# Performance work log

Hardware: AMD Instinct MI355X
Metric: run time of the kernel (lower is better)

## Reference

```python
import jax, jax.numpy as jnp
import numpy as np

B, N, CIN, H, UNITS = 8, 2048, 256, 256, 256


def setup_inputs() -> dict:
    key = jax.random.key(0)
    ks = jax.random.split(key, 7)
    s = 1.0 / np.sqrt(CIN)
    return {
        "x": jax.random.normal(ks[0], (B, N, CIN), dtype=jnp.float32),
        "Wq": jax.random.normal(ks[1], (CIN, H), dtype=jnp.float32) * s,
        "bq": jax.random.normal(ks[2], (H,), dtype=jnp.float32) * 0.01,
        "Wk": jax.random.normal(ks[3], (CIN, H), dtype=jnp.float32) * s,
        "bk": jax.random.normal(ks[4], (H,), dtype=jnp.float32) * 0.01,
        "Wm": jax.random.normal(ks[5], (H, UNITS), dtype=jnp.float32) * (1.0 / np.sqrt(H)),
        "bm": jax.random.normal(ks[6], (UNITS,), dtype=jnp.float32) * 0.01,
    }


def reference(x, Wq, bq, Wk, bk, Wm, bm):
    # Dense projections with fused relu (as in the Keras module)
    q = jax.nn.relu(x @ Wq + bq)          # (B,N,H)
    k = jax.nn.relu(x @ Wk + bk)          # (B,N,H)
    v = q                                 # NOTE: source uses fc_query for value (fc_value unused)
    # Unscaled key @ query^T, softmax over last axis
    kq = jax.nn.softmax(jnp.einsum('bnh,bmh->bnm', k, q), axis=-1)  # (B,N,N)
    # value^T @ kq, then Permute((2,1)): att[b,m,h] = sum_n v[b,n,h] * kq[b,n,m]
    att = jnp.einsum('bnh,bnm->bmh', v, kq)                          # (B,N,H)
    return jax.nn.relu(att @ Wm + bm)                                # (B,N,UNITS)
```

## Files before the change

### kernel.cpp

```cpp
#include <hip/hip_runtime.h>
#include <hip/hip_bf16.h>
#include <math.h>

#define BB   8
#define NN   2048
#define CC   256
#define MTOT (BB * NN)

typedef __bf16 bf16_t;
typedef bf16_t    bf16x8 __attribute__((ext_vector_type(8)));
typedef _Float16  halfx8 __attribute__((ext_vector_type(8)));
typedef float     floatx4 __attribute__((ext_vector_type(4)));

#define LOG2E 1.44269504088896f

__device__ __forceinline__ void gl_lds16(const bf16_t* g, bf16_t* l) {
    __builtin_amdgcn_global_load_lds(
        (const __attribute__((address_space(1))) unsigned int*)g,
        (__attribute__((address_space(3))) unsigned int*)l, 16, 0, 0);
}

template<int OMODE, bool BIASRELU, bool DO_STATS>
__global__ __launch_bounds__(256, 3)
void gemm_nt(const bf16_t* __restrict__ A, const bf16_t* __restrict__ B,
             void* __restrict__ C, const float* __restrict__ bias,
             int lda, int ldb, int ldc,
             long strideA, long strideB, long strideC,
             float* __restrict__ pm, float* __restrict__ pl)
{
    const int b = blockIdx.z;
    A += (long)b * strideA;
    B += (long)b * strideB;
    const int m0 = blockIdx.y * 128;
    const int n0 = blockIdx.x * 128;

    __shared__ bf16_t As[128 * 32];
    __shared__ bf16_t Bs[128 * 32];
    __shared__ float  smx[4][4][16];
    __shared__ float  ssm[4][4][16];

    const int tid  = threadIdx.x;
    const int wid  = tid >> 6, lane = tid & 63;
    const int wm   = (wid >> 1) * 64, wn = (wid & 1) * 64;
    const int fr   = lane & 15;
    const int kb   = (lane >> 4) * 8;

    floatx4 acc[4][4] = {};

    for (int k0 = 0; k0 < 256; k0 += 32) {
#pragma unroll
        for (int r = 0; r < 2; ++r) {
            const int lin = tid + r * 256;
            const int rw  = lin >> 2, kc = lin & 3;
            gl_lds16(A + (long)(m0 + rw) * lda + k0 + kc * 8, As + lin * 8);
            gl_lds16(B + (long)(n0 + rw) * ldb + k0 + kc * 8, Bs + lin * 8);
        }
        __syncthreads();
        bf16x8 af[4], bf[4];
#pragma unroll
        for (int f = 0; f < 4; ++f) {
            af[f] = *(const bf16x8*)(As + (wm + f * 16 + fr) * 32 + kb);
            bf[f] = *(const bf16x8*)(Bs + (wn + f * 16 + fr) * 32 + kb);
        }
#pragma unroll
        for (int f = 0; f < 4; ++f)
#pragma unroll
            for (int g = 0; g < 4; ++g)
                acc[f][g] = __builtin_amdgcn_mfma_f32_16x16x32_bf16(af[f], bf[g], acc[f][g], 0, 0, 0);
        __syncthreads();
    }

    const int rbase = (lane >> 4) * 4;
#pragma unroll
    for (int g = 0; g < 4; ++g) {
        const int n = n0 + wn + g * 16 + fr;
        const float bv = BIASRELU ? bias[n] : 0.0f;
#pragma unroll
        for (int f = 0; f < 4; ++f) {
#pragma unroll
            for (int r = 0; r < 4; ++r) {
                const int m = m0 + wm + f * 16 + rbase + r;
                float v = acc[f][g][r] + bv;
                if (BIASRELU) v = v > 0.0f ? v : 0.0f;
                if (OMODE == 0)
                    ((float*)C)[(long)b * strideC + (long)m * ldc + n] = v;
                else if (OMODE == 1)
                    ((bf16_t*)C)[(long)b * strideC + (long)m * ldc + n] = (bf16_t)v;
                else
                    ((_Float16*)C)[(long)b * strideC + (long)m * ldc + n] = (_Float16)v;
            }
        }
    }

    if (DO_STATS) {
        float lmax[4], lsum[4];
#pragma unroll
        for (int g = 0; g < 4; ++g) {
            float m = -1e30f;
#pragma unroll
            for (int f = 0; f < 4; ++f)
#pragma unroll
                for (int r = 0; r < 4; ++r) m = fmaxf(m, acc[f][g][r]);
            m = fmaxf(m, __shfl_xor(m, 16));
            m = fmaxf(m, __shfl_xor(m, 32));
            float s = 0.0f;
#pragma unroll
            for (int f = 0; f < 4; ++f)
#pragma unroll
                for (int r = 0; r < 4; ++r) s += __expf(acc[f][g][r] - m);
            s += __shfl_xor(s, 16);
            s += __shfl_xor(s, 32);
            lmax[g] = m; lsum[g] = s;
        }
        if (lane < 16) {
#pragma unroll
            for (int g = 0; g < 4; ++g) {
                smx[wid][g][lane] = lmax[g];
                ssm[wid][g][lane] = lsum[g];
            }
        }
        __syncthreads();
        if (tid < 128) {
            const int pair = tid >> 6;
            const int idx  = tid & 63;
            const int g = idx >> 4, f2 = idx & 15;
            const float m0v = smx[pair][g][f2], m1v = smx[pair + 2][g][f2];
            const float M = fmaxf(m0v, m1v);
            const float L = ssm[pair][g][f2] * __expf(m0v - M) +
                            ssm[pair + 2][g][f2] * __expf(m1v - M);
            const int n = n0 + pair * 64 + g * 16 + f2;
            const long o = ((long)b * 16 + blockIdx.y) * NN + n;
            pm[o] = M;
            pl[o] = L;
        }
    }
}

__global__ __launch_bounds__(256)
void stats_combine(const float* __restrict__ pm, const float* __restrict__ pl,
                   float* __restrict__ c2)
{
    const int i = blockIdx.x * 256 + threadIdx.x;
    const int b = i >> 11, n = i & 2047;
    float M = -1e30f, L = 0.0f;
#pragma unroll
    for (int t = 0; t < 16; ++t) {
        const long o = ((long)b * 16 + t) * NN + n;
        const float m = pm[o], l = pl[o];
        const float nm = fmaxf(M, m);
        L = L * __expf(M - nm) + l * __expf(m - nm);
        M = nm;
    }
    c2[i] = (M + logf(L)) * LOG2E;
}

#define APAD 68
__global__ __launch_bounds__(256, 4)
void att_out(const _Float16* __restrict__ St, const bf16_t* __restrict__ qmT,
             const float* __restrict__ c2, const float* __restrict__ bm,
             float* __restrict__ out)
{
    const int b  = blockIdx.z;
    const int m0 = blockIdx.x * 32;
    const int u0 = blockIdx.y * 128;
    const _Float16* S  = St  + (long)b * NN * NN;
    const bf16_t*   Q  = qmT + (long)b * 256 * NN;
    const float*    C2 = c2  + b * NN;
    float*          O  = out + (long)b * NN * 256;

    __shared__ bf16_t As[32 * APAD];
    __shared__ bf16_t Bs[128 * 64];

    const int tid  = threadIdx.x;
    const int wid  = tid >> 6, lane = tid & 63;
    const int wm2  = (wid >> 1) * 16;
    const int wu   = (wid & 1) * 64;
    const int fr   = lane & 15;
    const int u16  = lane >> 4;
    const int kb   = u16 * 8;
    const int fsw  = fr & 7;
    const int arow = tid >> 3;
    const int aseg = tid & 7;

    const _Float16* Srow = S + (long)(m0 + arow) * NN + aseg * 8;

    floatx4 acc[4] = {};

    for (int n0 = 0; n0 < NN; n0 += 64) {
#pragma unroll
        for (int r = 0; r < 4; ++r) {
            const int lin = tid + r * 256;
            const int rw  = lin >> 3, kc = lin & 7;
            const int kcs = kc ^ (rw & 7);
            gl_lds16(Q + (long)(u0 + rw) * NN + n0 + kcs * 8, Bs + lin * 8);
        }
        const halfx8 hv = *(const halfx8*)(Srow + n0);
        const float4 ca = *(const float4*)(C2 + n0 + aseg * 8);
        const float4 cb = *(const float4*)(C2 + n0 + aseg * 8 + 4);
        bf16x8 p;
        p[0] = (bf16_t)exp2f(fmaf((float)hv[0], LOG2E, -ca.x));
        p[1] = (bf16_t)exp2f(fmaf((float)hv[1], LOG2E, -ca.y));
        p[2] = (bf16_t)exp2f(fmaf((float)hv[2], LOG2E, -ca.z));
        p[3] = (bf16_t)exp2f(fmaf((float)hv[3], LOG2E, -ca.w));
        p[4] = (bf16_t)exp2f(fmaf((float)hv[4], LOG2E, -cb.x));
        p[5] = (bf16_t)exp2f(fmaf((float)hv[5], LOG2E, -cb.y));
        p[6] = (bf16_t)exp2f(fmaf((float)hv[6], LOG2E, -cb.z));
        p[7] = (bf16_t)exp2f(fmaf((float)hv[7], LOG2E, -cb.w));
        *(bf16x8*)(As + arow * APAD + aseg * 8) = p;
        __syncthreads();

        bf16x8 af[2], bg[4][2];
#pragma unroll
        for (int j = 0; j < 2; ++j)
            af[j] = *(const bf16x8*)(As + (wm2 + fr) * APAD + j * 32 + kb);
#pragma unroll
        for (int g = 0; g < 4; ++g)
#pragma unroll
            for (int j = 0; j < 2; ++j) {
                const int chunk = (j * 4 + u16) ^ fsw;
                bg[g][j] = *(const bf16x8*)(Bs + (wu + g * 16 + fr) * 64 + chunk * 8);
            }
#pragma unroll
        for (int j = 0; j < 2; ++j)
#pragma unroll
            for (int g = 0; g < 4; ++g)
                acc[g] = __builtin_amdgcn_mfma_f32_16x16x32_bf16(af[j], bg[g][j], acc[g], 0, 0, 0);
        __syncthreads();
    }

    const int rbase = u16 * 4;
#pragma unroll
    for (int g = 0; g < 4; ++g) {
        const int u = u0 + wu + g * 16 + fr;
        const float bvv = bm[u];
#pragma unroll
        for (int r = 0; r < 4; ++r) {
            const int m = m0 + wm2 + rbase + r;
            const float v = acc[g][r] + bvv;
            O[(long)m * 256 + u] = v > 0.0f ? v : 0.0f;
        }
    }
}

__global__ __launch_bounds__(256)
void cvt_bf16(const float* __restrict__ x, bf16_t* __restrict__ y)
{
    const long i = ((long)blockIdx.x * 256 + threadIdx.x) * 8;
    const float4 a = *(const float4*)(x + i);
    const float4 b = *(const float4*)(x + i + 4);
    bf16x8 o;
    o[0] = (bf16_t)a.x; o[1] = (bf16_t)a.y; o[2] = (bf16_t)a.z; o[3] = (bf16_t)a.w;
    o[4] = (bf16_t)b.x; o[5] = (bf16_t)b.y; o[6] = (bf16_t)b.z; o[7] = (bf16_t)b.w;
    *(bf16x8*)(y + i) = o;
}

__global__ __launch_bounds__(256)
void prep_w(const float* __restrict__ Wq, const float* __restrict__ Wk,
            const float* __restrict__ Wm, const float* __restrict__ bq,
            const float* __restrict__ bk, bf16_t* __restrict__ WqkT,
            bf16_t* __restrict__ WmT, float* __restrict__ bqk)
{
    const int z = blockIdx.z;
    const float* W = (z == 0) ? Wq : (z == 1) ? Wk : Wm;
    bf16_t* Wt = (z == 0) ? WqkT : (z == 1) ? (WqkT + 256 * 256) : WmT;
    __shared__ float t[32][33];
    const int n0 = blockIdx.x * 32, k0 = blockIdx.y * 32;
    const int tx = threadIdx.x & 31, ty = threadIdx.x >> 5;
    for (int i = ty; i < 32; i += 8) t[i][tx] = W[(k0 + i) * 256 + n0 + tx];
    __syncthreads();
    for (int i = ty; i < 32; i += 8) Wt[(n0 + i) * 256 + k0 + tx] = (bf16_t)t[tx][i];
    if (z == 0 && blockIdx.x == 0 && blockIdx.y == 0) {
        bqk[threadIdx.x]       = bq[threadIdx.x];
        bqk[256 + threadIdx.x] = bk[threadIdx.x];
    }
}

extern "C" void kernel_launch(void* const* d_in, const int* in_sizes, int n_in,
                              void* d_out, int out_size, void* d_ws, size_t ws_size,
                              hipStream_t stream)
{
    (void)in_sizes; (void)n_in; (void)out_size; (void)ws_size;
    const float* x  = (const float*)d_in[0];
    const float* Wq = (const float*)d_in[1];
    const float* bq = (const float*)d_in[2];
    const float* Wk = (const float*)d_in[3];
    const float* bk = (const float*)d_in[4];
    const float* Wm = (const float*)d_in[5];
    const float* bm = (const float*)d_in[6];
    float* out = (float*)d_out;

    char* w = (char*)d_ws;
    _Float16* St   = (_Float16*)w;                  w += (size_t)BB * NN * NN * 2;
    bf16_t* x_bf   = (bf16_t*)w;                    w += (size_t)MTOT * 256 * 2;
    bf16_t* qk     = (bf16_t*)w;                    w += (size_t)MTOT * 512 * 2;
    bf16_t* qmT    = (bf16_t*)w;                    w += (size_t)MTOT * 256 * 2;
    bf16_t* WqkT   = (bf16_t*)w;                    w += 512 * 256 * 2;
    bf16_t* WmT    = (bf16_t*)w;                    w += 256 * 256 * 2;
    float*  bqk    = (float*)w;                     w += 512 * 4;
    float*  pm     = (float*)w;                     w += (size_t)BB * 16 * NN * 4;
    float*  pl     = (float*)w;                     w += (size_t)BB * 16 * NN * 4;
    float*  c2b    = (float*)w;

    cvt_bf16<<<dim3(MTOT * 256 / (256 * 8)), 256, 0, stream>>>(x, x_bf);
    prep_w<<<dim3(8, 8, 3), 256, 0, stream>>>(Wq, Wk, Wm, bq, bk, WqkT, WmT, bqk);

    gemm_nt<1, true, false><<<dim3(4, 128, 1), 256, 0, stream>>>(
        x_bf, WqkT, qk, bqk, 256, 256, 512, 0, 0, 0, nullptr, nullptr);

    gemm_nt<1, false, false><<<dim3(16, 2, BB), 256, 0, stream>>>(
        WmT, qk, qmT, nullptr, 256, 512, NN,
        0, (long)NN * 512, (long)256 * NN, nullptr, nullptr);

    gemm_nt<2, false, true><<<dim3(16, 16, BB), 256, 0, stream>>>(
        qk, qk + 256, St, nullptr, 512, 512, NN,
        (long)NN * 512, (long)NN * 512, (long)NN * NN, pm, pl);

    stats_combine<<<dim3(MTOT / 256), 256, 0, stream>>>(pm, pl, c2b);

    att_out<<<dim3(64, 2, BB), 256, 0, stream>>>(St, qmT, c2b, bm, out);
}
```

Baseline: 179.6 us.

## Double-buffer att_out LDS tiles and double the row tile per block

New measurement: 184.8 us. 2.9% more time.

```diff
diff --git a/kernel.cpp b/kernel.cpp
--- a/kernel.cpp
+++ b/kernel.cpp
@@ -155,25 +155,25 @@
 }
 
 #define APAD 68
-__global__ __launch_bounds__(256, 4)
+__global__ __launch_bounds__(256, 3)
 void att_out(const _Float16* __restrict__ St, const bf16_t* __restrict__ qmT,
              const float* __restrict__ c2, const float* __restrict__ bm,
              float* __restrict__ out)
 {
     const int b  = blockIdx.z;
-    const int m0 = blockIdx.x * 32;
+    const int m0 = blockIdx.x * 64;
     const int u0 = blockIdx.y * 128;
     const _Float16* S  = St  + (long)b * NN * NN;
     const bf16_t*   Q  = qmT + (long)b * 256 * NN;
     const float*    C2 = c2  + b * NN;
     float*          O  = out + (long)b * NN * 256;
 
-    __shared__ bf16_t As[32 * APAD];
-    __shared__ bf16_t Bs[128 * 64];
+    __shared__ bf16_t As[2][64 * APAD];
+    __shared__ bf16_t Bs[2][128 * 64];
 
     const int tid  = threadIdx.x;
     const int wid  = tid >> 6, lane = tid & 63;
-    const int wm2  = (wid >> 1) * 16;
+    const int wm2  = (wid >> 1) * 32;
     const int wu   = (wid & 1) * 64;
     const int fr   = lane & 15;
     const int u16  = lane >> 4;
@@ -182,49 +182,85 @@
     const int arow = tid >> 3;
     const int aseg = tid & 7;
 
-    const _Float16* Srow = S + (long)(m0 + arow) * NN + aseg * 8;
-
-    floatx4 acc[4] = {};
-
-    for (int n0 = 0; n0 < NN; n0 += 64) {
+    const _Float16* S0 = S + (long)(m0 + arow) * NN + aseg * 8;
+    const _Float16* S1 = S0 + (long)32 * NN;
+    const float*    CA = C2 + aseg * 8;
+
+    floatx4 acc[2][4] = {};
+
+    halfx8 hv0, hv1;
+    float4 ca, cb;
+
+    auto loadA = [&](int n0) {
+        hv0 = *(const halfx8*)(S0 + n0);
+        hv1 = *(const halfx8*)(S1 + n0);
+        ca  = *(const float4*)(CA + n0);
+        cb  = *(const float4*)(CA + n0 + 4);
+    };
+    auto stageB = [&](int buf, int n0) {
 #pragma unroll
         for (int r = 0; r < 4; ++r) {
             const int lin = tid + r * 256;
             const int rw  = lin >> 3, kc = lin & 7;
             const int kcs = kc ^ (rw & 7);
-            gl_lds16(Q + (long)(u0 + rw) * NN + n0 + kcs * 8, Bs + lin * 8);
-        }
-        const halfx8 hv = *(const halfx8*)(Srow + n0);
-        const float4 ca = *(const float4*)(C2 + n0 + aseg * 8);
-        const float4 cb = *(const float4*)(C2 + n0 + aseg * 8 + 4);
-        bf16x8 p;
-        p[0] = (bf16_t)exp2f(fmaf((float)hv[0], LOG2E, -ca.x));
-        p[1] = (bf16_t)exp2f(fmaf((float)hv[1], LOG2E, -ca.y));
-        p[2] = (bf16_t)exp2f(fmaf((float)hv[2], LOG2E, -ca.z));
-        p[3] = (bf16_t)exp2f(fmaf((float)hv[3], LOG2E, -ca.w));
-        p[4] = (bf16_t)exp2f(fmaf((float)hv[4], LOG2E, -cb.x));
-        p[5] = (bf16_t)exp2f(fmaf((float)hv[5], LOG2E, -cb.y));
-        p[6] = (bf16_t)exp2f(fmaf((float)hv[6], LOG2E, -cb.z));
-        p[7] = (bf16_t)exp2f(fmaf((float)hv[7], LOG2E, -cb.w));
-        *(bf16x8*)(As + arow * APAD + aseg * 8) = p;
-        __syncthreads();
-
-        bf16x8 af[2], bg[4][2];
-#pragma unroll
-        for (int j = 0; j < 2; ++j)
-            af[j] = *(const bf16x8*)(As + (wm2 + fr) * APAD + j * 32 + kb);
+            gl_lds16(Q + (long)(u0 + rw) * NN + n0 + kcs * 8, &Bs[buf][lin * 8]);
+        }
+    };
+    auto packA = [&](int buf) {
+        bf16x8 p0, p1;
+        p0[0] = (bf16_t)exp2f(fmaf((float)hv0[0], LOG2E, -ca.x));
+        p0[1] = (bf16_t)exp2f(fmaf((float)hv0[1], LOG2E, -ca.y));
+        p0[2] = (bf16_t)exp2f(fmaf((float)hv0[2], LOG2E, -ca.z));
+        p0[3] = (bf16_t)exp2f(fmaf((float)hv0[3], LOG2E, -ca.w));
+        p0[4] = (bf16_t)exp2f(fmaf((float)hv0[4], LOG2E, -cb.x));
+        p0[5] = (bf16_t)exp2f(fmaf((float)hv0[5], LOG2E, -cb.y));
+        p0[6] = (bf16_t)exp2f(fmaf((float)hv0[6], LOG2E, -cb.z));
+        p0[7] = (bf16_t)exp2f(fmaf((float)hv0[7], LOG2E, -cb.w));
+        p1[0] = (bf16_t)exp2f(fmaf((float)hv1[0], LOG2E, -ca.x));
+        p1[1] = (bf16_t)exp2f(fmaf((float)hv1[1], LOG2E, -ca.y));
+        p1[2] = (bf16_t)exp2f(fmaf((float)hv1[2], LOG2E, -ca.z));
+        p1[3] = (bf16_t)exp2f(fmaf((float)hv1[3], LOG2E, -ca.w));
+        p1[4] = (bf16_t)exp2f(fmaf((float)hv1[4], LOG2E, -cb.x));
+        p1[5] = (bf16_t)exp2f(fmaf((float)hv1[5], LOG2E, -cb.y));
+        p1[6] = (bf16_t)exp2f(fmaf((float)hv1[6], LOG2E, -cb.z));
+        p1[7] = (bf16_t)exp2f(fmaf((float)hv1[7], LOG2E, -cb.w));
+        *(bf16x8*)(&As[buf][arow * APAD + aseg * 8])        = p0;
+        *(bf16x8*)(&As[buf][(arow + 32) * APAD + aseg * 8]) = p1;
+    };
+
+    loadA(0);
+    stageB(0, 0);
+    packA(0);
+    __syncthreads();
+
+    for (int it = 0; it < NN / 64; ++it) {
+        const int cur = it & 1;
+        if (it + 1 < NN / 64) {
+            loadA((it + 1) * 64);
+            stageB(cur ^ 1, (it + 1) * 64);
+        }
+        bf16x8 af[2][2], bg[4][2];
+#pragma unroll
+        for (int f = 0; f < 2; ++f)
+#pragma unroll
+            for (int j = 0; j < 2; ++j)
+                af[f][j] = *(const bf16x8*)(&As[cur][(wm2 + f * 16 + fr) * APAD + j * 32 + kb]);
 #pragma unroll
         for (int g = 0; g < 4; ++g)
 #pragma unroll
             for (int j = 0; j < 2; ++j) {
                 const int chunk = (j * 4 + u16) ^ fsw;
-                bg[g][j] = *(const bf16x8*)(Bs + (wu + g * 16 + fr) * 64 + chunk * 8);
+                bg[g][j] = *(const bf16x8*)(&Bs[cur][(wu + g * 16 + fr) * 64 + chunk * 8]);
             }
 #pragma unroll
         for (int j = 0; j < 2; ++j)
 #pragma unroll
-            for (int g = 0; g < 4; ++g)
-                acc[g] = __builtin_amdgcn_mfma_f32_16x16x32_bf16(af[j], bg[g][j], acc[g], 0, 0, 0);
+            for (int f = 0; f < 2; ++f)
+#pragma unroll
+                for (int g = 0; g < 4; ++g)
+                    acc[f][g] = __builtin_amdgcn_mfma_f32_16x16x32_bf16(af[f][j], bg[g][j], acc[f][g], 0, 0, 0);
+        if (it + 1 < NN / 64)
+            packA(cur ^ 1);
         __syncthreads();
     }
 
@@ -234,11 +270,13 @@
         const int u = u0 + wu + g * 16 + fr;
         const float bvv = bm[u];
 #pragma unroll
-        for (int r = 0; r < 4; ++r) {
-            const int m = m0 + wm2 + rbase + r;
-            const float v = acc[g][r] + bvv;
-            O[(long)m * 256 + u] = v > 0.0f ? v : 0.0f;
-        }
+        for (int f = 0; f < 2; ++f)
+#pragma unroll
+            for (int r = 0; r < 4; ++r) {
+                const int m = m0 + wm2 + f * 16 + rbase + r;
+                const float v = acc[f][g][r] + bvv;
+                O[(long)m * 256 + u] = v > 0.0f ? v : 0.0f;
+            }
     }
 }
 
@@ -317,5 +355,5 @@
 
     stats_combine<<<dim3(MTOT / 256), 256, 0, stream>>>(pm, pl, c2b);
 
-    att_out<<<dim3(64, 2, BB), 256, 0, stream>>>(St, qmT, c2b, bm, out);
-}
+    att_out<<<dim3(32, 2, BB), 256, 0, stream>>>(St, qmT, c2b, bm, out);
+}
```

## Pipeline att_out with triple-buffered B tiles and a larger 64-row M tile

Applied to the files above, without the earlier changes.

Result: slower. 199.2 us (+10.9%).

```diff
diff --git a/kernel.cpp b/kernel.cpp
--- a/kernel.cpp
+++ b/kernel.cpp
@@ -155,25 +155,99 @@
 }
 
 #define APAD 68
-__global__ __launch_bounds__(256, 4)
+
+#define LA_(t, s) { \
+    hA0_##s = *(const halfx8*)(S0 + (long)(t) * 64); \
+    hA1_##s = *(const halfx8*)(S1 + (long)(t) * 64); \
+    cA_##s  = *(const float4*)(CA + (t) * 64); \
+    cB_##s  = *(const float4*)(CA + (t) * 64 + 4); }
+
+#define SB_(bufofs, t) { \
+    _Pragma("unroll") \
+    for (int r = 0; r < 4; ++r) { \
+        const int lin = tid + r * 256; \
+        const int rw = lin >> 3, kc = lin & 7; \
+        const int kcs = kc ^ (rw & 7); \
+        gl_lds16(Q + (long)(u0 + rw) * NN + (t) * 64 + kcs * 8, \
+                 Bs + (bufofs) + lin * 8); } }
+
+#define PACKA_(aofs, s) { \
+    bf16x8 p0, p1; \
+    p0[0] = (bf16_t)exp2f(fmaf((float)hA0_##s[0], LOG2E, -cA_##s.x)); \
+    p0[1] = (bf16_t)exp2f(fmaf((float)hA0_##s[1], LOG2E, -cA_##s.y)); \
+    p0[2] = (bf16_t)exp2f(fmaf((float)hA0_##s[2], LOG2E, -cA_##s.z)); \
+    p0[3] = (bf16_t)exp2f(fmaf((float)hA0_##s[3], LOG2E, -cA_##s.w)); \
+    p0[4] = (bf16_t)exp2f(fmaf((float)hA0_##s[4], LOG2E, -cB_##s.x)); \
+    p0[5] = (bf16_t)exp2f(fmaf((float)hA0_##s[5], LOG2E, -cB_##s.y)); \
+    p0[6] = (bf16_t)exp2f(fmaf((float)hA0_##s[6], LOG2E, -cB_##s.z)); \
+    p0[7] = (bf16_t)exp2f(fmaf((float)hA0_##s[7], LOG2E, -cB_##s.w)); \
+    p1[0] = (bf16_t)exp2f(fmaf((float)hA1_##s[0], LOG2E, -cA_##s.x)); \
+    p1[1] = (bf16_t)exp2f(fmaf((float)hA1_##s[1], LOG2E, -cA_##s.y)); \
+    p1[2] = (bf16_t)exp2f(fmaf((float)hA1_##s[2], LOG2E, -cA_##s.z)); \
+    p1[3] = (bf16_t)exp2f(fmaf((float)hA1_##s[3], LOG2E, -cA_##s.w)); \
+    p1[4] = (bf16_t)exp2f(fmaf((float)hA1_##s[4], LOG2E, -cB_##s.x)); \
+    p1[5] = (bf16_t)exp2f(fmaf((float)hA1_##s[5], LOG2E, -cB_##s.y)); \
+    p1[6] = (bf16_t)exp2f(fmaf((float)hA1_##s[6], LOG2E, -cB_##s.z)); \
+    p1[7] = (bf16_t)exp2f(fmaf((float)hA1_##s[7], LOG2E, -cB_##s.w)); \
+    *(bf16x8*)(As + (aofs) + arow * APAD + aseg * 8)        = p0; \
+    *(bf16x8*)(As + (aofs) + (arow + 32) * APAD + aseg * 8) = p1; }
+
+#define ITER_(it, sI, sP) { \
+    const int t2 = (it) + 2 < 32 ? (it) + 2 : 31; \
+    LA_(t2, sI); \
+    SB_(bstg * 8192, t2); \
+    const bf16_t* asr = As + ((it) & 1) * (64 * APAD); \
+    const bf16_t* bsr = Bs + bcur * 8192; \
+    bf16x8 af[2][2], bg[4][2]; \
+    _Pragma("unroll") \
+    for (int f = 0; f < 2; ++f) \
+        _Pragma("unroll") \
+        for (int j = 0; j < 2; ++j) \
+            af[f][j] = *(const bf16x8*)(asr + (wm2 + f * 16 + fr) * APAD + j * 32 + kb); \
+    _Pragma("unroll") \
+    for (int g = 0; g < 4; ++g) \
+        _Pragma("unroll") \
+        for (int j = 0; j < 2; ++j) { \
+            const int chunk = (j * 4 + u16) ^ fsw; \
+            bg[g][j] = *(const bf16x8*)(bsr + (wu + g * 16 + fr) * 64 + chunk * 8); \
+        } \
+    asm volatile("s_waitcnt lgkmcnt(0)" ::: "memory"); \
+    __builtin_amdgcn_sched_barrier(0); \
+    __builtin_amdgcn_s_setprio(1); \
+    _Pragma("unroll") \
+    for (int j = 0; j < 2; ++j) \
+        _Pragma("unroll") \
+        for (int f = 0; f < 2; ++f) \
+            _Pragma("unroll") \
+            for (int g = 0; g < 4; ++g) \
+                acc[f][g] = __builtin_amdgcn_mfma_f32_16x16x32_bf16(af[f][j], bg[g][j], acc[f][g], 0, 0, 0); \
+    __builtin_amdgcn_s_setprio(0); \
+    PACKA_((((it) + 1) & 1) * (64 * APAD), sP); \
+    asm volatile("s_waitcnt vmcnt(8) lgkmcnt(0)" ::: "memory"); \
+    __builtin_amdgcn_sched_barrier(0); \
+    __builtin_amdgcn_s_barrier(); \
+    bcur = bcur == 2 ? 0 : bcur + 1; \
+    bstg = bstg == 2 ? 0 : bstg + 1; }
+
+__global__ __launch_bounds__(256, 2)
 void att_out(const _Float16* __restrict__ St, const bf16_t* __restrict__ qmT,
              const float* __restrict__ c2, const float* __restrict__ bm,
              float* __restrict__ out)
 {
     const int b  = blockIdx.z;
-    const int m0 = blockIdx.x * 32;
+    const int m0 = blockIdx.x * 64;
     const int u0 = blockIdx.y * 128;
     const _Float16* S  = St  + (long)b * NN * NN;
     const bf16_t*   Q  = qmT + (long)b * 256 * NN;
     const float*    C2 = c2  + b * NN;
     float*          O  = out + (long)b * NN * 256;
 
-    __shared__ bf16_t As[32 * APAD];
-    __shared__ bf16_t Bs[128 * 64];
+    __shared__ bf16_t As[2 * 64 * APAD];
+    __shared__ bf16_t Bs[3 * 128 * 64];
 
     const int tid  = threadIdx.x;
     const int wid  = tid >> 6, lane = tid & 63;
-    const int wm2  = (wid >> 1) * 16;
+    const int wm2  = (wid >> 1) * 32;
     const int wu   = (wid & 1) * 64;
     const int fr   = lane & 15;
     const int u16  = lane >> 4;
@@ -182,50 +256,28 @@
     const int arow = tid >> 3;
     const int aseg = tid & 7;
 
-    const _Float16* Srow = S + (long)(m0 + arow) * NN + aseg * 8;
-
-    floatx4 acc[4] = {};
-
-    for (int n0 = 0; n0 < NN; n0 += 64) {
-#pragma unroll
-        for (int r = 0; r < 4; ++r) {
-            const int lin = tid + r * 256;
-            const int rw  = lin >> 3, kc = lin & 7;
-            const int kcs = kc ^ (rw & 7);
-            gl_lds16(Q + (long)(u0 + rw) * NN + n0 + kcs * 8, Bs + lin * 8);
-        }
-        const halfx8 hv = *(const halfx8*)(Srow + n0);
-        const float4 ca = *(const float4*)(C2 + n0 + aseg * 8);
-        const float4 cb = *(const float4*)(C2 + n0 + aseg * 8 + 4);
-        bf16x8 p;
-        p[0] = (bf16_t)exp2f(fmaf((float)hv[0], LOG2E, -ca.x));
-        p[1] = (bf16_t)exp2f(fmaf((float)hv[1], LOG2E, -ca.y));
-        p[2] = (bf16_t)exp2f(fmaf((float)hv[2], LOG2E, -ca.z));
-        p[3] = (bf16_t)exp2f(fmaf((float)hv[3], LOG2E, -ca.w));
-        p[4] = (bf16_t)exp2f(fmaf((float)hv[4], LOG2E, -cb.x));
-        p[5] = (bf16_t)exp2f(fmaf((float)hv[5], LOG2E, -cb.y));
-        p[6] = (bf16_t)exp2f(fmaf((float)hv[6], LOG2E, -cb.z));
-        p[7] = (bf16_t)exp2f(fmaf((float)hv[7], LOG2E, -cb.w));
-        *(bf16x8*)(As + arow * APAD + aseg * 8) = p;
-        __syncthreads();
-
-        bf16x8 af[2], bg[4][2];
-#pragma unroll
-        for (int j = 0; j < 2; ++j)
-            af[j] = *(const bf16x8*)(As + (wm2 + fr) * APAD + j * 32 + kb);
-#pragma unroll
-        for (int g = 0; g < 4; ++g)
-#pragma unroll
-            for (int j = 0; j < 2; ++j) {
-                const int chunk = (j * 4 + u16) ^ fsw;
-                bg[g][j] = *(const bf16x8*)(Bs + (wu + g * 16 + fr) * 64 + chunk * 8);
-            }
-#pragma unroll
-        for (int j = 0; j < 2; ++j)
-#pragma unroll
-            for (int g = 0; g < 4; ++g)
-                acc[g] = __builtin_amdgcn_mfma_f32_16x16x32_bf16(af[j], bg[g][j], acc[g], 0, 0, 0);
-        __syncthreads();
+    const _Float16* S0 = S + (long)(m0 + arow) * NN + aseg * 8;
+    const _Float16* S1 = S0 + (long)32 * NN;
+    const float*    CA = C2 + aseg * 8;
+
+    floatx4 acc[2][4] = {};
+
+    halfx8 hA0_0, hA1_0, hA0_1, hA1_1;
+    float4 cA_0, cB_0, cA_1, cB_1;
+    int bcur = 0, bstg = 2;
+
+    LA_(0, 0);
+    SB_(0, 0);
+    LA_(1, 1);
+    SB_(8192, 1);
+    PACKA_(0, 0);
+    asm volatile("s_waitcnt vmcnt(8) lgkmcnt(0)" ::: "memory");
+    __builtin_amdgcn_sched_barrier(0);
+    __builtin_amdgcn_s_barrier();
+
+    for (int it = 0; it < 32; it += 2) {
+        ITER_(it, 0, 1);
+        ITER_(it + 1, 1, 0);
     }
 
     const int rbase = u16 * 4;
@@ -234,11 +286,13 @@
         const int u = u0 + wu + g * 16 + fr;
         const float bvv = bm[u];
 #pragma unroll
-        for (int r = 0; r < 4; ++r) {
-            const int m = m0 + wm2 + rbase + r;
-            const float v = acc[g][r] + bvv;
-            O[(long)m * 256 + u] = v > 0.0f ? v : 0.0f;
-        }
+        for (int f = 0; f < 2; ++f)
+#pragma unroll
+            for (int r = 0; r < 4; ++r) {
+                const int m = m0 + wm2 + f * 16 + rbase + r;
+                const float v = acc[f][g][r] + bvv;
+                O[(long)m * 256 + u] = v > 0.0f ? v : 0.0f;
+            }
     }
 }
 
@@ -317,5 +371,5 @@
 
     stats_combine<<<dim3(MTOT / 256), 256, 0, stream>>>(pm, pl, c2b);
 
-    att_out<<<dim3(64, 2, BB), 256, 0, stream>>>(St, qmT, c2b, bm, out);
-}
+    att_out<<<dim3(32, 2, BB), 256, 0, stream>>>(St, qmT, c2b, bm, out);
+}
```

## Pipeline att_out with register-direct B loads and double-buffered P tile

Applied to the files above, without the earlier changes.

Result: slower. 264.7 us (+47.4%).

```diff
diff --git a/kernel.cpp b/kernel.cpp
--- a/kernel.cpp
+++ b/kernel.cpp
@@ -155,7 +155,51 @@
 }
 
 #define APAD 68
-__global__ __launch_bounds__(256, 4)
+
+#define LAV_(s, t) { \
+    hv_##s = *(const halfx8*)(S0 + (long)(t) * 64); \
+    ca_##s = *(const float4*)(CA + (t) * 64); \
+    cb_##s = *(const float4*)(CA + (t) * 64 + 4); }
+
+#define LBV_(s, t) { \
+    _Pragma("unroll") \
+    for (int g = 0; g < 4; ++g) { \
+        bga_##s[g] = *(const bf16x8*)(Qb + (long)g * 16 * NN + (long)(t) * 64); \
+        bgb_##s[g] = *(const bf16x8*)(Qb + (long)g * 16 * NN + (long)(t) * 64 + 32); } }
+
+#define PACKV_(s, bufidx) { \
+    bf16x8 p; \
+    p[0] = (bf16_t)exp2f(fmaf((float)hv_##s[0], LOG2E, -ca_##s.x)); \
+    p[1] = (bf16_t)exp2f(fmaf((float)hv_##s[1], LOG2E, -ca_##s.y)); \
+    p[2] = (bf16_t)exp2f(fmaf((float)hv_##s[2], LOG2E, -ca_##s.z)); \
+    p[3] = (bf16_t)exp2f(fmaf((float)hv_##s[3], LOG2E, -ca_##s.w)); \
+    p[4] = (bf16_t)exp2f(fmaf((float)hv_##s[4], LOG2E, -cb_##s.x)); \
+    p[5] = (bf16_t)exp2f(fmaf((float)hv_##s[5], LOG2E, -cb_##s.y)); \
+    p[6] = (bf16_t)exp2f(fmaf((float)hv_##s[6], LOG2E, -cb_##s.z)); \
+    p[7] = (bf16_t)exp2f(fmaf((float)hv_##s[7], LOG2E, -cb_##s.w)); \
+    *(bf16x8*)(&As[bufidx][arow * APAD + aseg * 8]) = p; }
+
+#define MMV_(s, bufidx) { \
+    bf16x8 af0 = *(const bf16x8*)(&As[bufidx][(wmw + fr) * APAD + kb]); \
+    bf16x8 af1 = *(const bf16x8*)(&As[bufidx][(wmw + fr) * APAD + 32 + kb]); \
+    _Pragma("unroll") \
+    for (int g = 0; g < 4; ++g) \
+        acc[g] = __builtin_amdgcn_mfma_f32_16x16x32_bf16(af0, bga_##s[g], acc[g], 0, 0, 0); \
+    _Pragma("unroll") \
+    for (int g = 0; g < 4; ++g) \
+        acc[g] = __builtin_amdgcn_mfma_f32_16x16x32_bf16(af1, bgb_##s[g], acc[g], 0, 0, 0); }
+
+#define ITERV_(t, p, q) { \
+    const int tn1 = (t) + 1 < 32 ? (t) + 1 : 31; \
+    const int tn2 = (t) + 2 < 32 ? (t) + 2 : 31; \
+    LAV_(p, tn2); \
+    LBV_(q, tn1); \
+    MMV_(p, (t) & 1); \
+    PACKV_(q, ((t) + 1) & 1); \
+    asm volatile("s_waitcnt lgkmcnt(0)" ::: "memory"); \
+    __builtin_amdgcn_s_barrier(); }
+
+__global__ __launch_bounds__(256, 3)
 void att_out(const _Float16* __restrict__ St, const bf16_t* __restrict__ qmT,
              const float* __restrict__ c2, const float* __restrict__ bm,
              float* __restrict__ out)
@@ -168,64 +212,38 @@
     const float*    C2 = c2  + b * NN;
     float*          O  = out + (long)b * NN * 256;
 
-    __shared__ bf16_t As[32 * APAD];
-    __shared__ bf16_t Bs[128 * 64];
+    __shared__ bf16_t As[2][32 * APAD];
 
     const int tid  = threadIdx.x;
     const int wid  = tid >> 6, lane = tid & 63;
-    const int wm2  = (wid >> 1) * 16;
+    const int wmw  = (wid >> 1) * 16;
     const int wu   = (wid & 1) * 64;
     const int fr   = lane & 15;
     const int u16  = lane >> 4;
     const int kb   = u16 * 8;
-    const int fsw  = fr & 7;
     const int arow = tid >> 3;
     const int aseg = tid & 7;
 
-    const _Float16* Srow = S + (long)(m0 + arow) * NN + aseg * 8;
+    const _Float16* S0 = S + (long)(m0 + arow) * NN + aseg * 8;
+    const float*    CA = C2 + aseg * 8;
+    const bf16_t*   Qb = Q + (long)(u0 + wu + fr) * NN + kb;
 
     floatx4 acc[4] = {};
 
-    for (int n0 = 0; n0 < NN; n0 += 64) {
-#pragma unroll
-        for (int r = 0; r < 4; ++r) {
-            const int lin = tid + r * 256;
-            const int rw  = lin >> 3, kc = lin & 7;
-            const int kcs = kc ^ (rw & 7);
-            gl_lds16(Q + (long)(u0 + rw) * NN + n0 + kcs * 8, Bs + lin * 8);
-        }
-        const halfx8 hv = *(const halfx8*)(Srow + n0);
-        const float4 ca = *(const float4*)(C2 + n0 + aseg * 8);
-        const float4 cb = *(const float4*)(C2 + n0 + aseg * 8 + 4);
-        bf16x8 p;
-        p[0] = (bf16_t)exp2f(fmaf((float)hv[0], LOG2E, -ca.x));
-        p[1] = (bf16_t)exp2f(fmaf((float)hv[1], LOG2E, -ca.y));
-        p[2] = (bf16_t)exp2f(fmaf((float)hv[2], LOG2E, -ca.z));
-        p[3] = (bf16_t)exp2f(fmaf((float)hv[3], LOG2E, -ca.w));
-        p[4] = (bf16_t)exp2f(fmaf((float)hv[4], LOG2E, -cb.x));
-        p[5] = (bf16_t)exp2f(fmaf((float)hv[5], LOG2E, -cb.y));
-        p[6] = (bf16_t)exp2f(fmaf((float)hv[6], LOG2E, -cb.z));
-        p[7] = (bf16_t)exp2f(fmaf((float)hv[7], LOG2E, -cb.w));
-        *(bf16x8*)(As + arow * APAD + aseg * 8) = p;
-        __syncthreads();
-
-        bf16x8 af[2], bg[4][2];
-#pragma unroll
-        for (int j = 0; j < 2; ++j)
-            af[j] = *(const bf16x8*)(As + (wm2 + fr) * APAD + j * 32 + kb);
-#pragma unroll
-        for (int g = 0; g < 4; ++g)
-#pragma unroll
-            for (int j = 0; j < 2; ++j) {
-                const int chunk = (j * 4 + u16) ^ fsw;
-                bg[g][j] = *(const bf16x8*)(Bs + (wu + g * 16 + fr) * 64 + chunk * 8);
-            }
-#pragma unroll
-        for (int j = 0; j < 2; ++j)
-#pragma unroll
-            for (int g = 0; g < 4; ++g)
-                acc[g] = __builtin_amdgcn_mfma_f32_16x16x32_bf16(af[j], bg[g][j], acc[g], 0, 0, 0);
-        __syncthreads();
+    halfx8 hv_0, hv_1;
+    float4 ca_0, cb_0, ca_1, cb_1;
+    bf16x8 bga_0[4], bgb_0[4], bga_1[4], bgb_1[4];
+
+    LAV_(0, 0);
+    LBV_(0, 0);
+    LAV_(1, 1);
+    PACKV_(0, 0);
+    asm volatile("s_waitcnt lgkmcnt(0)" ::: "memory");
+    __builtin_amdgcn_s_barrier();
+
+    for (int t = 0; t < 32; t += 2) {
+        ITERV_(t, 0, 1);
+        ITERV_(t + 1, 1, 0);
     }
 
     const int rbase = u16 * 4;
@@ -235,7 +253,7 @@
         const float bvv = bm[u];
 #pragma unroll
         for (int r = 0; r < 4; ++r) {
-            const int m = m0 + wm2 + rbase + r;
+            const int m = m0 + wmw + rbase + r;
             const float v = acc[g][r] + bvv;
             O[(long)m * 256 + u] = v > 0.0f ? v : 0.0f;
         }
```
